# Kernel tuning notes

Measured on AMD Instinct MI355X. Metric: run time of the kernel, lower is better.

## Reference

```python
import jax, jax.numpy as jnp
import numpy as np

B, S, D = 8, 4096, 512
Q, C = 8, 1024


def setup_inputs() -> dict:
    key = jax.random.key(0)
    kx, kc = jax.random.split(key)
    x = jax.random.normal(kx, (B, S, D), dtype=jnp.float32)
    # learned codebooks for each residual quantizer level: [Q, C, D]
    codebooks = jax.random.normal(kc, (Q, C, D), dtype=jnp.float32)
    return {"x": x, "codebooks": codebooks}


def reference(x, codebooks):
    """Residual VQ: cascaded nearest-codebook lookups over residuals.

    Returns (quantized_out, indices [B,S,Q], commit_losses [Q]).
    """

    def step(carry, cb):
        residual, quant_out = carry
        # squared-distance argmin; ||r||^2 term is constant over codes, drop it
        # dist[b,s,c] ~ ||cb_c||^2 - 2 <r_bs, cb_c>
        dist = jnp.sum(cb * cb, axis=-1) - 2.0 * jnp.einsum("bsd,cd->bsc", residual, cb)
        idx = jnp.argmin(dist, axis=-1)            # [B, S]
        q = cb[idx]                                 # [B, S, D] gather
        commit = jnp.mean((jax.lax.stop_gradient(q) - residual) ** 2)
        # straight-through estimator
        q_st = residual + jax.lax.stop_gradient(q - residual)
        new_residual = residual - jax.lax.stop_gradient(q)
        return (new_residual, quant_out + q_st), (idx, commit)

    init = (x, jnp.zeros_like(x))
    (_, quantized), (indices, losses) = jax.lax.scan(step, init, codebooks)
    indices = jnp.transpose(indices, (1, 2, 0))  # [B, S, Q]
    return quantized, indices, losses
```

## Files before the change

### kernel.cpp

```cpp
#include <hip/hip_runtime.h>

#define BD 8
#define SD 4096
#define DDIM 512
#define QD 8
#define CDN 1024
#define ROWS (BD * SD)
#define QUANT_ELEMS (ROWS * DDIM)
#define IDX_OFF QUANT_ELEMS
#define LOSS_OFF (QUANT_ELEMS + ROWS * QD)

#define TPB 256
#define BR 32
#define MARGIN 0.25f

#define WS_LOSS 0
#define WS_FBCNT 64
#define WS_FBLIST 4096
#define WS_NORMS 0x40000
#define WS_PKHI 0x100000
#define WS_PKLO 0x900000
#define WS_RESID 0x1100000

typedef __attribute__((ext_vector_type(8))) short short8;
typedef __attribute__((ext_vector_type(4))) float f32x4;

__device__ __forceinline__ ushort f2bf(float x) {
    unsigned u = __float_as_uint(x);
    u += 0x7fff + ((u >> 16) & 1);
    return (ushort)(u >> 16);
}

__global__ __launch_bounds__(256) void vq_norms(const float* __restrict__ cb,
                                                float* __restrict__ norms) {
    int code = blockIdx.x * 4 + (threadIdx.x >> 6);
    int lane = threadIdx.x & 63;
    const float4* p = (const float4*)(cb + (size_t)code * DDIM);
    float4 a = p[lane];
    float4 b = p[lane + 64];
    float s = a.x * a.x + a.y * a.y + a.z * a.z + a.w * a.w +
              b.x * b.x + b.y * b.y + b.z * b.z + b.w * b.w;
#pragma unroll
    for (int m = 32; m >= 1; m >>= 1) s += __shfl_xor(s, m);
    if (lane == 0) norms[code] = s;
}

__global__ __launch_bounds__(256) void vq_cbpack(const float* __restrict__ cbs,
                                                 ushort* __restrict__ pkHi,
                                                 ushort* __restrict__ pkLo) {
    int sg = blockIdx.x * 256 + threadIdx.x;
    int lvl = sg >> 16;
    int s = sg & 65535;
    int tile = s >> 10;
    int kc = (s >> 6) & 15;
    int ln = s & 63;
    int code = tile * 16 + (ln & 15);
    int k0 = kc * 32 + (ln >> 4) * 8;
    const float* p = cbs + (size_t)lvl * CDN * DDIM + (size_t)code * DDIM + k0;
    float f[8];
    *(float4*)&f[0] = *(const float4*)p;
    *(float4*)&f[4] = *(const float4*)(p + 4);
    ushort h[8], l[8];
#pragma unroll
    for (int i = 0; i < 8; i++) {
        h[i] = f2bf(f[i]);
        float hf = __uint_as_float(((unsigned)h[i]) << 16);
        l[i] = f2bf(f[i] - hf);
    }
    *(short8*)(pkHi + (size_t)sg * 8) = *(short8*)h;
    *(short8*)(pkLo + (size_t)sg * 8) = *(short8*)l;
}

__global__ __launch_bounds__(TPB, 2) void vq_level_mfma(
    const float* __restrict__ rsrc, const float* __restrict__ qsub,
    float* __restrict__ resid, float* __restrict__ quant,
    const float* __restrict__ cbq, const float* __restrict__ normq,
    const ushort* __restrict__ pkHi, const ushort* __restrict__ pkLo,
    float* __restrict__ idx_out, double* __restrict__ lossq,
    int* __restrict__ fbCnt, int* __restrict__ fbList, int q) {
    __shared__ ushort Ah[BR * 512];
    __shared__ ushort Al[BR * 512];
    __shared__ float s_nrm[CDN];
    __shared__ float m_d1[4][BR], m_d2[4][BR], m_d3[4][BR];
    __shared__ int m_i1[4][BR], m_i2[4][BR];
    __shared__ int s_i1[BR], s_i2[BR], s_flag[BR];
    __shared__ double s_part[4];

    int tid = threadIdx.x;
    int lane = tid & 63;
    int l15 = lane & 15;
    int quad = lane >> 4;
    int cg = tid >> 6;
    int row0 = blockIdx.x * BR;

    for (int i = tid; i < CDN; i += TPB) s_nrm[i] = normq[i];

#pragma unroll
    for (int i = 0; i < 8; i++) {
        int flat = tid + TPB * i;
        int row = flat >> 6;
        int c = flat & 63;
        size_t g = (size_t)(row0 + row) * DDIM + c * 8;
        float f[8];
        *(float4*)&f[0] = *(const float4*)(rsrc + g);
        *(float4*)&f[4] = *(const float4*)(rsrc + g + 4);
        if (qsub) {
            float4 w0 = *(const float4*)(qsub + g);
            float4 w1 = *(const float4*)(qsub + g + 4);
            f[0] -= w0.x; f[1] -= w0.y; f[2] -= w0.z; f[3] -= w0.w;
            f[4] -= w1.x; f[5] -= w1.y; f[6] -= w1.z; f[7] -= w1.w;
        }
        ushort h[8], l[8];
#pragma unroll
        for (int k = 0; k < 8; k++) {
            h[k] = f2bf(f[k]);
            float hf = __uint_as_float(((unsigned)h[k]) << 16);
            l[k] = f2bf(f[k] - hf);
        }
        int dst = row * 512 + ((c ^ (row & 7)) * 8);
        *(short8*)(Ah + dst) = *(short8*)h;
        *(short8*)(Al + dst) = *(short8*)l;
    }
    __syncthreads();

    float td1[8], td2[8], td3[8];
    int ti1[8], ti2[8];
#pragma unroll
    for (int s = 0; s < 8; s++) { td1[s] = 3.4e38f; td2[s] = 3.4e38f; td3[s] = 3.4e38f; ti1[s] = 0; ti2[s] = 0; }

    short8 aR[2][4], bhR[2][4], blR[2][4];
    f32x4 acc[2][4];
    int aswz = l15 & 7;

#define LOADB(g, p) { int ct_ = (g) >> 4, kc_ = (g) & 15; \
    int base_ = ct_ * 131072 + cg * 32768 + kc_ * 512 + lane * 8; \
    _Pragma("unroll") for (int j = 0; j < 4; j++) { \
        bhR[p][j] = *(const short8*)(pkHi + base_ + j * 8192); \
        blR[p][j] = *(const short8*)(pkLo + base_ + j * 8192); } }

#define LOADA(g, p) { int c0_ = (((g) & 15) * 4 + quad) ^ aswz; \
    aR[p][0] = *(short8*)(Ah + l15 * 512 + c0_ * 8); \
    aR[p][1] = *(short8*)(Al + l15 * 512 + c0_ * 8); \
    aR[p][2] = *(short8*)(Ah + (16 + l15) * 512 + c0_ * 8); \
    aR[p][3] = *(short8*)(Al + (16 + l15) * 512 + c0_ * 8); }

#define BODY(g, p) { \
    if (((g) & 15) == 0) { \
        _Pragma("unroll") for (int rt = 0; rt < 2; rt++) \
        _Pragma("unroll") for (int j = 0; j < 4; j++) acc[rt][j] = (f32x4)0.0f; } \
    if ((g) < 63) { LOADB((g) + 1, 1 - (p)); LOADA((g) + 1, 1 - (p)); } \
    _Pragma("unroll") for (int j = 0; j < 4; j++) { \
        acc[0][j] = __builtin_amdgcn_mfma_f32_16x16x32_bf16(aR[p][0], bhR[p][j], acc[0][j], 0, 0, 0); \
        acc[0][j] = __builtin_amdgcn_mfma_f32_16x16x32_bf16(aR[p][1], bhR[p][j], acc[0][j], 0, 0, 0); \
        acc[0][j] = __builtin_amdgcn_mfma_f32_16x16x32_bf16(aR[p][0], blR[p][j], acc[0][j], 0, 0, 0); \
        acc[1][j] = __builtin_amdgcn_mfma_f32_16x16x32_bf16(aR[p][2], bhR[p][j], acc[1][j], 0, 0, 0); \
        acc[1][j] = __builtin_amdgcn_mfma_f32_16x16x32_bf16(aR[p][3], bhR[p][j], acc[1][j], 0, 0, 0); \
        acc[1][j] = __builtin_amdgcn_mfma_f32_16x16x32_bf16(aR[p][2], blR[p][j], acc[1][j], 0, 0, 0); } \
    if (((g) & 15) == 15) { int ct_ = (g) >> 4; \
        _Pragma("unroll") for (int j = 0; j < 4; j++) { \
            int code = (ct_ * 16 + cg * 4 + j) * 16 + l15; \
            float nrm = s_nrm[code]; \
            _Pragma("unroll") for (int rt = 0; rt < 2; rt++) \
            _Pragma("unroll") for (int reg = 0; reg < 4; reg++) { \
                float v = nrm - 2.0f * acc[rt][j][reg]; \
                int s = rt * 4 + reg; \
                bool b1 = v < td1[s]; bool b2 = v < td2[s]; bool b3 = v < td3[s]; \
                td3[s] = b2 ? td2[s] : (b3 ? v : td3[s]); \
                ti2[s] = b1 ? ti1[s] : (b2 ? code : ti2[s]); \
                td2[s] = b1 ? td1[s] : (b2 ? v : td2[s]); \
                ti1[s] = b1 ? code : ti1[s]; \
                td1[s] = b1 ? v : td1[s]; } } } }

    LOADB(0, 0); LOADA(0, 0);
    for (int gp = 0; gp < 32; gp++) {
        int g0 = gp * 2;
        BODY(g0, 0);
        BODY(g0 + 1, 1);
    }
#undef LOADB
#undef LOADA
#undef BODY

#pragma unroll
    for (int m = 1; m <= 8; m <<= 1) {
#pragma unroll
        for (int s = 0; s < 8; s++) {
            float o1 = __shfl_xor(td1[s], m); int oi1 = __shfl_xor(ti1[s], m);
            float o2 = __shfl_xor(td2[s], m); int oi2 = __shfl_xor(ti2[s], m);
            float o3 = __shfl_xor(td3[s], m);
            bool aw = (td1[s] < o1) || (td1[s] == o1 && ti1[s] < oi1);
            float w2 = aw ? td2[s] : o2; int wi2 = aw ? ti2[s] : oi2;
            float w3 = aw ? td3[s] : o3;
            float n1 = aw ? td1[s] : o1; int ni1 = aw ? ti1[s] : oi1;
            float p1 = aw ? o1 : td1[s]; int pi1 = aw ? oi1 : ti1[s];
            float p2 = aw ? o2 : td2[s];
            bool sw = (w2 < p1) || (w2 == p1 && wi2 < pi1);
            float n2 = sw ? w2 : p1; int ni2 = sw ? wi2 : pi1;
            float n3 = sw ? fminf(p1, w3) : fminf(w2, p2);
            td1[s] = n1; ti1[s] = ni1; td2[s] = n2; ti2[s] = ni2; td3[s] = n3;
        }
    }

    if (l15 == 0) {
#pragma unroll
        for (int s = 0; s < 8; s++) {
            int row = (s >> 2) * 16 + quad * 4 + (s & 3);
            m_d1[cg][row] = td1[s]; m_i1[cg][row] = ti1[s];
            m_d2[cg][row] = td2[s]; m_i2[cg][row] = ti2[s];
            m_d3[cg][row] = td3[s];
        }
    }
    __syncthreads();

    if (tid < BR) {
        int r = tid;
        float d1 = m_d1[0][r]; int i1 = m_i1[0][r];
        float d2 = m_d2[0][r]; int i2 = m_i2[0][r];
        float d3 = m_d3[0][r];
#pragma unroll
        for (int c = 1; c < 4; c++) {
            float o1 = m_d1[c][r]; int oi1 = m_i1[c][r];
            float o2 = m_d2[c][r]; int oi2 = m_i2[c][r];
            float o3 = m_d3[c][r];
            bool aw = (d1 < o1) || (d1 == o1 && i1 < oi1);
            float w2 = aw ? d2 : o2; int wi2 = aw ? i2 : oi2;
            float w3 = aw ? d3 : o3;
            float n1 = aw ? d1 : o1; int ni1 = aw ? i1 : oi1;
            float p1 = aw ? o1 : d1; int pi1 = aw ? oi1 : i1;
            float p2 = aw ? o2 : d2;
            bool sw = (w2 < p1) || (w2 == p1 && wi2 < pi1);
            float n2 = sw ? w2 : p1; int ni2 = sw ? wi2 : pi1;
            float n3 = sw ? fminf(p1, w3) : fminf(w2, p2);
            d1 = n1; i1 = ni1; d2 = n2; i2 = ni2; d3 = n3;
        }
        int flag = 0;
        if (d3 - d1 < MARGIN) flag = 2;
        else if (d2 - d1 < MARGIN) flag = 1;
        s_i1[r] = i1; s_i2[r] = i2; s_flag[r] = flag;
        if (flag == 2) {
            int p = atomicAdd(fbCnt, 1);
            if (p < 32768) fbList[p] = row0 + r;
        }
    }
    __syncthreads();

    for (int r = cg; r < BR; r += 4) {
        if (s_flag[r] != 1) continue;
        int i1 = s_i1[r], i2 = s_i2[r];
        size_t g = (size_t)(row0 + r) * DDIM + lane * 8;
        float rv[8];
        *(float4*)&rv[0] = *(const float4*)(rsrc + g);
        *(float4*)&rv[4] = *(const float4*)(rsrc + g + 4);
        if (qsub) {
            float4 w0 = *(const float4*)(qsub + g);
            float4 w1 = *(const float4*)(qsub + g + 4);
            rv[0] -= w0.x; rv[1] -= w0.y; rv[2] -= w0.z; rv[3] -= w0.w;
            rv[4] -= w1.x; rv[5] -= w1.y; rv[6] -= w1.z; rv[7] -= w1.w;
        }
        float c1[8], c2[8];
        *(float4*)&c1[0] = *(const float4*)(cbq + (size_t)i1 * DDIM + lane * 8);
        *(float4*)&c1[4] = *(const float4*)(cbq + (size_t)i1 * DDIM + lane * 8 + 4);
        *(float4*)&c2[0] = *(const float4*)(cbq + (size_t)i2 * DDIM + lane * 8);
        *(float4*)&c2[4] = *(const float4*)(cbq + (size_t)i2 * DDIM + lane * 8 + 4);
        float e1 = 0.0f, e2 = 0.0f;
#pragma unroll
        for (int i = 0; i < 8; i++) { e1 = fmaf(rv[i], c1[i], e1); e2 = fmaf(rv[i], c2[i], e2); }
#pragma unroll
        for (int m = 32; m >= 1; m >>= 1) { e1 += __shfl_xor(e1, m); e2 += __shfl_xor(e2, m); }
        float dd1 = s_nrm[i1] - 2.0f * e1;
        float dd2 = s_nrm[i2] - 2.0f * e2;
        bool take2 = (dd2 < dd1) || (dd2 == dd1 && i2 < i1);
        if (lane == 0) s_i1[r] = take2 ? i2 : i1;
    }
    __syncthreads();

    if (tid < BR) idx_out[(size_t)(row0 + tid) * QD + q] = (float)s_i1[tid];

    double ls = 0.0;
#pragma unroll 4
    for (int it = 0; it < 16; it++) {
        int flat = tid + TPB * it;
        int row = flat >> 7;
        int c4 = (flat & 127) * 4;
        if (s_flag[row] == 2) continue;
        size_t g = (size_t)(row0 + row) * DDIM + c4;
        float4 r = *(const float4*)(rsrc + g);
        if (qsub) {
            float4 w = *(const float4*)(qsub + g);
            r.x -= w.x; r.y -= w.y; r.z -= w.z; r.w -= w.w;
        }
        float4 cv = *(const float4*)(cbq + (size_t)s_i1[row] * DDIM + c4);
        float4 nr;
        nr.x = r.x - cv.x; nr.y = r.y - cv.y; nr.z = r.z - cv.z; nr.w = r.w - cv.w;
        if (resid) {
            *(float4*)(resid + g) = nr;
        } else {
            float4 qo = *(float4*)(quant + g);
            qo.x += cv.x; qo.y += cv.y; qo.z += cv.z; qo.w += cv.w;
            *(float4*)(quant + g) = qo;
        }
        ls += (double)nr.x * nr.x + (double)nr.y * nr.y +
              (double)nr.z * nr.z + (double)nr.w * nr.w;
    }
#pragma unroll
    for (int m = 32; m >= 1; m >>= 1) ls += __shfl_down(ls, m);
    if ((tid & 63) == 0) s_part[tid >> 6] = ls;
    __syncthreads();
    if (tid == 0) {
        double t = s_part[0] + s_part[1] + s_part[2] + s_part[3];
        atomicAdd(lossq, t);
    }
}

__global__ __launch_bounds__(256) void vq_fallback(
    const float* __restrict__ rsrc, const float* __restrict__ qsub,
    float* __restrict__ resid, float* __restrict__ quant,
    const float* __restrict__ cbq, const float* __restrict__ normq,
    float* __restrict__ idx_out, double* __restrict__ lossq,
    const int* __restrict__ fbCnt, const int* __restrict__ fbList, int q) {
    __shared__ float r_s[DDIM];
    __shared__ unsigned long long s_best;
    int tid = threadIdx.x;
    int n = *fbCnt; if (n > 32768) n = 32768;
    for (int w = blockIdx.x; w < n; w += gridDim.x) {
        int row = fbList[w];
        if (tid == 0) s_best = ~0ull;
        if (tid < 128) {
            size_t g = (size_t)row * DDIM + tid * 4;
            float4 v = *(const float4*)(rsrc + g);
            if (qsub) {
                float4 x = *(const float4*)(qsub + g);
                v.x -= x.x; v.y -= x.y; v.z -= x.z; v.w -= x.w;
            }
            *(float4*)&r_s[tid * 4] = v;
        }
        __syncthreads();
#pragma unroll
        for (int cc = 0; cc < 4; cc++) {
            int c = tid + 256 * cc;
            float dot = 0.0f;
            for (int k4 = 0; k4 < 128; k4++) {
                float4 cv = *(const float4*)(cbq + (size_t)c * DDIM + k4 * 4);
                float4 rv = *(const float4*)&r_s[k4 * 4];
                dot = fmaf(cv.x, rv.x, dot); dot = fmaf(cv.y, rv.y, dot);
                dot = fmaf(cv.z, rv.z, dot); dot = fmaf(cv.w, rv.w, dot);
            }
            float dist = normq[c] - 2.0f * dot;
            unsigned b = __float_as_uint(dist);
            b = (b & 0x80000000u) ? ~b : (b | 0x80000000u);
            unsigned long long key = (((unsigned long long)b) << 32) | (unsigned)c;
            atomicMin(&s_best, key);
        }
        __syncthreads();
        int idx = (int)(s_best & 0xffffffffull);
        if (tid == 0) idx_out[(size_t)row * QD + q] = (float)idx;
        double ls = 0.0;
        if (tid < 128) {
            size_t g = (size_t)row * DDIM + tid * 4;
            float4 r = *(const float4*)&r_s[tid * 4];
            float4 cv = *(const float4*)(cbq + (size_t)idx * DDIM + tid * 4);
            float4 nr;
            nr.x = r.x - cv.x; nr.y = r.y - cv.y; nr.z = r.z - cv.z; nr.w = r.w - cv.w;
            if (resid) {
                *(float4*)(resid + g) = nr;
            } else {
                float4 qo = *(float4*)(quant + g);
                qo.x += cv.x; qo.y += cv.y; qo.z += cv.z; qo.w += cv.w;
                *(float4*)(quant + g) = qo;
            }
            ls = (double)nr.x * nr.x + (double)nr.y * nr.y +
                 (double)nr.z * nr.z + (double)nr.w * nr.w;
        }
#pragma unroll
        for (int m = 32; m >= 1; m >>= 1) ls += __shfl_down(ls, m);
        if ((tid & 63) == 0 && ls != 0.0) atomicAdd(lossq, ls);
        __syncthreads();
    }
}

__global__ __launch_bounds__(256) void vq_quant_final(const float* __restrict__ x,
                                                      const float* __restrict__ resid,
                                                      float* __restrict__ quant) {
    size_t i = ((size_t)blockIdx.x * 256 + threadIdx.x) * 4;
    float4 xv = *(const float4*)(x + i);
    float4 rv = *(const float4*)(resid + i);
    float4 o;
    o.x = xv.x - rv.x; o.y = xv.y - rv.y; o.z = xv.z - rv.z; o.w = xv.w - rv.w;
    *(float4*)(quant + i) = o;
}

__global__ void vq_loss_final(const double* __restrict__ lossws, float* __restrict__ out) {
    int i = threadIdx.x;
    if (i < QD) out[i] = (float)(lossws[i] * (1.0 / (double)((size_t)ROWS * DDIM)));
}

extern "C" void kernel_launch(void* const* d_in, const int* in_sizes, int n_in,
                              void* d_out, int out_size, void* d_ws, size_t ws_size,
                              hipStream_t stream) {
    const float* x = (const float*)d_in[0];
    const float* cbs = (const float*)d_in[1];
    float* out = (float*)d_out;
    float* quant = out;
    float* idxo = out + IDX_OFF;
    float* losso = out + LOSS_OFF;

    char* ws = (char*)d_ws;
    double* lossws = (double*)(ws + WS_LOSS);
    int* fbCnt = (int*)(ws + WS_FBCNT);
    int* fbList = (int*)(ws + WS_FBLIST);
    float* norms = (float*)(ws + WS_NORMS);
    ushort* pkHi = (ushort*)(ws + WS_PKHI);
    ushort* pkLo = (ushort*)(ws + WS_PKLO);
    float* resid = (ws_size >= (size_t)WS_RESID + (size_t)QUANT_ELEMS * 4)
                       ? (float*)(ws + WS_RESID) : nullptr;

    hipMemsetAsync(d_ws, 0, 128, stream);
    if (!resid) hipMemsetAsync(d_out, 0, (size_t)out_size * 4, stream);

    vq_norms<<<QD * CDN / 4, 256, 0, stream>>>(cbs, norms);
    vq_cbpack<<<QD * 256, 256, 0, stream>>>(cbs, pkHi, pkLo);

    for (int q = 0; q < QD; q++) {
        const float* cbq = cbs + (size_t)q * CDN * DDIM;
        const float* nq = norms + (size_t)q * CDN;
        const ushort* pH = pkHi + (size_t)q * CDN * DDIM;
        const ushort* pL = pkLo + (size_t)q * CDN * DDIM;
        const float* rsrc;
        const float* qsubA;
        if (resid) {
            rsrc = (q == 0) ? x : resid;
            qsubA = nullptr;
        } else {
            rsrc = x;
            qsubA = quant;
        }
        vq_level_mfma<<<ROWS / BR, TPB, 0, stream>>>(
            rsrc, qsubA, resid, quant, cbq, nq, pH, pL,
            idxo, lossws + q, fbCnt + q, fbList, q);
        vq_fallback<<<128, 256, 0, stream>>>(
            rsrc, qsubA, resid, quant, cbq, nq, idxo, lossws + q,
            fbCnt + q, fbList, q);
    }
    if (resid) {
        vq_quant_final<<<QUANT_ELEMS / 1024, 256, 0, stream>>>(x, resid, quant);
    }
    vq_loss_final<<<1, 64, 0, stream>>>(lossws, losso);
}
```

Before: 1.784 ms.

## Use 8 waves per block and restructure MFMA loop over all code tiles

Doubles the block to 512 threads (8 waves), so each wave now covers half as many codes per tile. The main loop becomes K-outer over all four code tiles, keeping accumulators for every tile live and running the top-3 selection once at the end instead of per tile. This cuts B-operand loads per wave and reloads A fragments less often, aiming for more waves in flight and better latency hiding. In exchange it holds more accumulator registers, and the launch bound now asks for 4 blocks of 512 threads, which may force spills or limit occupancy.

After: 2.237 ms. 25.4% more time.

```diff
diff --git a/kernel.cpp b/kernel.cpp
--- a/kernel.cpp
+++ b/kernel.cpp
@@ -10,7 +10,8 @@
 #define IDX_OFF QUANT_ELEMS
 #define LOSS_OFF (QUANT_ELEMS + ROWS * QD)
 
-#define TPB 256
+#define TPB 512
+#define NWAVE (TPB / 64)
 #define BR 32
 #define MARGIN 0.25f
 
@@ -71,7 +72,7 @@
     *(short8*)(pkLo + (size_t)sg * 8) = *(short8*)l;
 }
 
-__global__ __launch_bounds__(TPB, 2) void vq_level_mfma(
+__global__ __launch_bounds__(TPB, 4) void vq_level_mfma(
     const float* __restrict__ rsrc, const float* __restrict__ qsub,
     float* __restrict__ resid, float* __restrict__ quant,
     const float* __restrict__ cbq, const float* __restrict__ normq,
@@ -81,10 +82,10 @@
     __shared__ ushort Ah[BR * 512];
     __shared__ ushort Al[BR * 512];
     __shared__ float s_nrm[CDN];
-    __shared__ float m_d1[4][BR], m_d2[4][BR], m_d3[4][BR];
-    __shared__ int m_i1[4][BR], m_i2[4][BR];
+    __shared__ float m_d1[NWAVE][BR], m_d2[NWAVE][BR], m_d3[NWAVE][BR];
+    __shared__ int m_i1[NWAVE][BR], m_i2[NWAVE][BR];
     __shared__ int s_i1[BR], s_i2[BR], s_flag[BR];
-    __shared__ double s_part[4];
+    __shared__ double s_part[NWAVE];
 
     int tid = threadIdx.x;
     int lane = tid & 63;
@@ -96,7 +97,7 @@
     for (int i = tid; i < CDN; i += TPB) s_nrm[i] = normq[i];
 
 #pragma unroll
-    for (int i = 0; i < 8; i++) {
+    for (int i = 0; i < 2048 / TPB; i++) {
         int flat = tid + TPB * i;
         int row = flat >> 6;
         int c = flat & 63;
@@ -128,58 +129,78 @@
 #pragma unroll
     for (int s = 0; s < 8; s++) { td1[s] = 3.4e38f; td2[s] = 3.4e38f; td3[s] = 3.4e38f; ti1[s] = 0; ti2[s] = 0; }
 
-    short8 aR[2][4], bhR[2][4], blR[2][4];
-    f32x4 acc[2][4];
+    short8 aR[2][4], bhR[2][2], blR[2][2];
+    f32x4 acc[2][4][2];
+#pragma unroll
+    for (int rt = 0; rt < 2; rt++)
+#pragma unroll
+        for (int ct = 0; ct < 4; ct++)
+#pragma unroll
+            for (int j = 0; j < 2; j++) acc[rt][ct][j] = (f32x4)0.0f;
     int aswz = l15 & 7;
 
-#define LOADB(g, p) { int ct_ = (g) >> 4, kc_ = (g) & 15; \
-    int base_ = ct_ * 131072 + cg * 32768 + kc_ * 512 + lane * 8; \
-    _Pragma("unroll") for (int j = 0; j < 4; j++) { \
-        bhR[p][j] = *(const short8*)(pkHi + base_ + j * 8192); \
-        blR[p][j] = *(const short8*)(pkLo + base_ + j * 8192); } }
-
-#define LOADA(g, p) { int c0_ = (((g) & 15) * 4 + quad) ^ aswz; \
+#define LOADB(g, p) { int kc_ = (g) >> 2, ct_ = (g) & 3; \
+    int base_ = ct_ * 131072 + cg * 16384 + kc_ * 512 + lane * 8; \
+    bhR[p][0] = *(const short8*)(pkHi + base_); \
+    blR[p][0] = *(const short8*)(pkLo + base_); \
+    bhR[p][1] = *(const short8*)(pkHi + base_ + 8192); \
+    blR[p][1] = *(const short8*)(pkLo + base_ + 8192); }
+
+#define LOADA(kc, p) { int c0_ = ((kc) * 4 + quad) ^ aswz; \
     aR[p][0] = *(short8*)(Ah + l15 * 512 + c0_ * 8); \
     aR[p][1] = *(short8*)(Al + l15 * 512 + c0_ * 8); \
     aR[p][2] = *(short8*)(Ah + (16 + l15) * 512 + c0_ * 8); \
     aR[p][3] = *(short8*)(Al + (16 + l15) * 512 + c0_ * 8); }
 
-#define BODY(g, p) { \
-    if (((g) & 15) == 0) { \
-        _Pragma("unroll") for (int rt = 0; rt < 2; rt++) \
-        _Pragma("unroll") for (int j = 0; j < 4; j++) acc[rt][j] = (f32x4)0.0f; } \
-    if ((g) < 63) { LOADB((g) + 1, 1 - (p)); LOADA((g) + 1, 1 - (p)); } \
-    _Pragma("unroll") for (int j = 0; j < 4; j++) { \
-        acc[0][j] = __builtin_amdgcn_mfma_f32_16x16x32_bf16(aR[p][0], bhR[p][j], acc[0][j], 0, 0, 0); \
-        acc[0][j] = __builtin_amdgcn_mfma_f32_16x16x32_bf16(aR[p][1], bhR[p][j], acc[0][j], 0, 0, 0); \
-        acc[0][j] = __builtin_amdgcn_mfma_f32_16x16x32_bf16(aR[p][0], blR[p][j], acc[0][j], 0, 0, 0); \
-        acc[1][j] = __builtin_amdgcn_mfma_f32_16x16x32_bf16(aR[p][2], bhR[p][j], acc[1][j], 0, 0, 0); \
-        acc[1][j] = __builtin_amdgcn_mfma_f32_16x16x32_bf16(aR[p][3], bhR[p][j], acc[1][j], 0, 0, 0); \
-        acc[1][j] = __builtin_amdgcn_mfma_f32_16x16x32_bf16(aR[p][2], blR[p][j], acc[1][j], 0, 0, 0); } \
-    if (((g) & 15) == 15) { int ct_ = (g) >> 4; \
-        _Pragma("unroll") for (int j = 0; j < 4; j++) { \
-            int code = (ct_ * 16 + cg * 4 + j) * 16 + l15; \
-            float nrm = s_nrm[code]; \
-            _Pragma("unroll") for (int rt = 0; rt < 2; rt++) \
-            _Pragma("unroll") for (int reg = 0; reg < 4; reg++) { \
-                float v = nrm - 2.0f * acc[rt][j][reg]; \
-                int s = rt * 4 + reg; \
-                bool b1 = v < td1[s]; bool b2 = v < td2[s]; bool b3 = v < td3[s]; \
-                td3[s] = b2 ? td2[s] : (b3 ? v : td3[s]); \
-                ti2[s] = b1 ? ti1[s] : (b2 ? code : ti2[s]); \
-                td2[s] = b1 ? td1[s] : (b2 ? v : td2[s]); \
-                ti1[s] = b1 ? code : ti1[s]; \
-                td1[s] = b1 ? v : td1[s]; } } } }
-
-    LOADB(0, 0); LOADA(0, 0);
-    for (int gp = 0; gp < 32; gp++) {
-        int g0 = gp * 2;
-        BODY(g0, 0);
-        BODY(g0 + 1, 1);
+#define STEP(g, CT, BP, AP, PA, kcA, apA) { \
+    LOADB((g) + 1, 1 - (BP)); \
+    if (PA) LOADA(kcA, apA); \
+    _Pragma("unroll") for (int j = 0; j < 2; j++) { \
+        acc[0][CT][j] = __builtin_amdgcn_mfma_f32_16x16x32_bf16(aR[AP][0], bhR[BP][j], acc[0][CT][j], 0, 0, 0); \
+        acc[0][CT][j] = __builtin_amdgcn_mfma_f32_16x16x32_bf16(aR[AP][1], bhR[BP][j], acc[0][CT][j], 0, 0, 0); \
+        acc[0][CT][j] = __builtin_amdgcn_mfma_f32_16x16x32_bf16(aR[AP][0], blR[BP][j], acc[0][CT][j], 0, 0, 0); \
+        acc[1][CT][j] = __builtin_amdgcn_mfma_f32_16x16x32_bf16(aR[AP][2], bhR[BP][j], acc[1][CT][j], 0, 0, 0); \
+        acc[1][CT][j] = __builtin_amdgcn_mfma_f32_16x16x32_bf16(aR[AP][3], bhR[BP][j], acc[1][CT][j], 0, 0, 0); \
+        acc[1][CT][j] = __builtin_amdgcn_mfma_f32_16x16x32_bf16(aR[AP][2], blR[BP][j], acc[1][CT][j], 0, 0, 0); } }
+
+    LOADB(0, 0);
+    LOADA(0, 0);
+    for (int kc2 = 0; kc2 < 8; kc2++) {
+        int g0 = kc2 * 8;
+        int nl = (kc2 < 7);
+        STEP(g0 + 0, 0, 0, 0, 1, 2 * kc2 + 1, 1);
+        STEP(g0 + 1, 1, 1, 0, 0, 0, 0);
+        STEP(g0 + 2, 2, 0, 0, 0, 0, 0);
+        STEP(g0 + 3, 3, 1, 0, 0, 0, 0);
+        STEP(g0 + 4, 0, 0, 1, nl, 2 * kc2 + 2, 0);
+        STEP(g0 + 5, 1, 1, 1, 0, 0, 0);
+        STEP(g0 + 6, 2, 0, 1, 0, 0, 0);
+        STEP(g0 + 7, 3, 1, 1, 0, 0, 0);
     }
 #undef LOADB
 #undef LOADA
-#undef BODY
+#undef STEP
+
+#pragma unroll
+    for (int ct = 0; ct < 4; ct++)
+#pragma unroll
+        for (int jj = 0; jj < 2; jj++) {
+            int code = (ct * 16 + cg * 2 + jj) * 16 + l15;
+            float nrm = s_nrm[code];
+#pragma unroll
+            for (int rt = 0; rt < 2; rt++)
+#pragma unroll
+                for (int reg = 0; reg < 4; reg++) {
+                    float v = nrm - 2.0f * acc[rt][ct][jj][reg];
+                    int s = rt * 4 + reg;
+                    bool b1 = v < td1[s]; bool b2 = v < td2[s]; bool b3 = v < td3[s];
+                    td3[s] = b2 ? td2[s] : (b3 ? v : td3[s]);
+                    ti2[s] = b1 ? ti1[s] : (b2 ? code : ti2[s]);
+                    td2[s] = b1 ? td1[s] : (b2 ? v : td2[s]);
+                    ti1[s] = b1 ? code : ti1[s];
+                    td1[s] = b1 ? v : td1[s];
+                }
+        }
 
 #pragma unroll
     for (int m = 1; m <= 8; m <<= 1) {
@@ -218,7 +239,7 @@
         float d2 = m_d2[0][r]; int i2 = m_i2[0][r];
         float d3 = m_d3[0][r];
 #pragma unroll
-        for (int c = 1; c < 4; c++) {
+        for (int c = 1; c < NWAVE; c++) {
             float o1 = m_d1[c][r]; int oi1 = m_i1[c][r];
             float o2 = m_d2[c][r]; int oi2 = m_i2[c][r];
             float o3 = m_d3[c][r];
@@ -244,7 +265,7 @@
     }
     __syncthreads();
 
-    for (int r = cg; r < BR; r += 4) {
+    for (int r = cg; r < BR; r += NWAVE) {
         if (s_flag[r] != 1) continue;
         int i1 = s_i1[r], i2 = s_i2[r];
         size_t g = (size_t)(row0 + r) * DDIM + lane * 8;
@@ -278,7 +299,7 @@
 
     double ls = 0.0;
 #pragma unroll 4
-    for (int it = 0; it < 16; it++) {
+    for (int it = 0; it < 4096 / TPB; it++) {
         int flat = tid + TPB * it;
         int row = flat >> 7;
         int c4 = (flat & 127) * 4;
@@ -307,7 +328,9 @@
     if ((tid & 63) == 0) s_part[tid >> 6] = ls;
     __syncthreads();
     if (tid == 0) {
-        double t = s_part[0] + s_part[1] + s_part[2] + s_part[3];
+        double t = 0.0;
+#pragma unroll
+        for (int i = 0; i < NWAVE; i++) t += s_part[i];
         atomicAdd(lossq, t);
     }
 }
```

## Replace split-bf16 triple MFMA with single fp16 MFMA and widen fallback margin

Applied to the files above, without the earlier changes.

Replaces the three-pass hi/lo bf16 MFMA distance computation with one fp16 MFMA pass. This cuts matrix work, codebook bandwidth and LDS footprint to roughly a third, and drops the lo-part packing. To absorb the larger fp16 rounding error, the near-tie margin that triggers exact fp32 re-checks rises from 0.25 to 0.75, so more rows go through the verification and fallback paths. The top-2 indices are also packed into one register per slot to lower register pressure.

Result: faster. 1.498 ms (-16.0%).

```diff
diff --git a/kernel.cpp b/kernel.cpp
--- a/kernel.cpp
+++ b/kernel.cpp
@@ -11,25 +11,20 @@
 #define LOSS_OFF (QUANT_ELEMS + ROWS * QD)
 
 #define TPB 256
+#define NWAVE (TPB / 64)
 #define BR 32
-#define MARGIN 0.25f
+#define MARGIN 0.75f
 
 #define WS_LOSS 0
 #define WS_FBCNT 64
 #define WS_FBLIST 4096
 #define WS_NORMS 0x40000
-#define WS_PKHI 0x100000
-#define WS_PKLO 0x900000
+#define WS_PK 0x100000
 #define WS_RESID 0x1100000
 
 typedef __attribute__((ext_vector_type(8))) short short8;
+typedef __attribute__((ext_vector_type(8))) _Float16 half8;
 typedef __attribute__((ext_vector_type(4))) float f32x4;
-
-__device__ __forceinline__ ushort f2bf(float x) {
-    unsigned u = __float_as_uint(x);
-    u += 0x7fff + ((u >> 16) & 1);
-    return (ushort)(u >> 16);
-}
 
 __global__ __launch_bounds__(256) void vq_norms(const float* __restrict__ cb,
                                                 float* __restrict__ norms) {
@@ -46,8 +41,7 @@
 }
 
 __global__ __launch_bounds__(256) void vq_cbpack(const float* __restrict__ cbs,
-                                                 ushort* __restrict__ pkHi,
-                                                 ushort* __restrict__ pkLo) {
+                                                 ushort* __restrict__ pk) {
     int sg = blockIdx.x * 256 + threadIdx.x;
     int lvl = sg >> 16;
     int s = sg & 65535;
@@ -60,31 +54,25 @@
     float f[8];
     *(float4*)&f[0] = *(const float4*)p;
     *(float4*)&f[4] = *(const float4*)(p + 4);
-    ushort h[8], l[8];
-#pragma unroll
-    for (int i = 0; i < 8; i++) {
-        h[i] = f2bf(f[i]);
-        float hf = __uint_as_float(((unsigned)h[i]) << 16);
-        l[i] = f2bf(f[i] - hf);
-    }
-    *(short8*)(pkHi + (size_t)sg * 8) = *(short8*)h;
-    *(short8*)(pkLo + (size_t)sg * 8) = *(short8*)l;
+    _Float16 h[8];
+#pragma unroll
+    for (int i = 0; i < 8; i++) h[i] = (_Float16)f[i];
+    *(short8*)(pk + (size_t)sg * 8) = *(short8*)h;
 }
 
 __global__ __launch_bounds__(TPB, 2) void vq_level_mfma(
     const float* __restrict__ rsrc, const float* __restrict__ qsub,
     float* __restrict__ resid, float* __restrict__ quant,
     const float* __restrict__ cbq, const float* __restrict__ normq,
-    const ushort* __restrict__ pkHi, const ushort* __restrict__ pkLo,
+    const ushort* __restrict__ pk,
     float* __restrict__ idx_out, double* __restrict__ lossq,
     int* __restrict__ fbCnt, int* __restrict__ fbList, int q) {
     __shared__ ushort Ah[BR * 512];
-    __shared__ ushort Al[BR * 512];
     __shared__ float s_nrm[CDN];
-    __shared__ float m_d1[4][BR], m_d2[4][BR], m_d3[4][BR];
-    __shared__ int m_i1[4][BR], m_i2[4][BR];
+    __shared__ float m_d1[NWAVE][BR], m_d2[NWAVE][BR], m_d3[NWAVE][BR];
+    __shared__ int m_i1[NWAVE][BR], m_i2[NWAVE][BR];
     __shared__ int s_i1[BR], s_i2[BR], s_flag[BR];
-    __shared__ double s_part[4];
+    __shared__ double s_part[NWAVE];
 
     int tid = threadIdx.x;
     int lane = tid & 63;
@@ -110,39 +98,31 @@
             f[0] -= w0.x; f[1] -= w0.y; f[2] -= w0.z; f[3] -= w0.w;
             f[4] -= w1.x; f[5] -= w1.y; f[6] -= w1.z; f[7] -= w1.w;
         }
-        ushort h[8], l[8];
-#pragma unroll
-        for (int k = 0; k < 8; k++) {
-            h[k] = f2bf(f[k]);
-            float hf = __uint_as_float(((unsigned)h[k]) << 16);
-            l[k] = f2bf(f[k] - hf);
-        }
+        _Float16 h[8];
+#pragma unroll
+        for (int k = 0; k < 8; k++) h[k] = (_Float16)f[k];
         int dst = row * 512 + ((c ^ (row & 7)) * 8);
         *(short8*)(Ah + dst) = *(short8*)h;
-        *(short8*)(Al + dst) = *(short8*)l;
     }
     __syncthreads();
 
     float td1[8], td2[8], td3[8];
-    int ti1[8], ti2[8];
-#pragma unroll
-    for (int s = 0; s < 8; s++) { td1[s] = 3.4e38f; td2[s] = 3.4e38f; td3[s] = 3.4e38f; ti1[s] = 0; ti2[s] = 0; }
-
-    short8 aR[2][4], bhR[2][4], blR[2][4];
+    int t12[8];
+#pragma unroll
+    for (int s = 0; s < 8; s++) { td1[s] = 3.4e38f; td2[s] = 3.4e38f; td3[s] = 3.4e38f; t12[s] = 0; }
+
+    half8 aR[2][2], bR[2][4];
     f32x4 acc[2][4];
     int aswz = l15 & 7;
 
 #define LOADB(g, p) { int ct_ = (g) >> 4, kc_ = (g) & 15; \
     int base_ = ct_ * 131072 + cg * 32768 + kc_ * 512 + lane * 8; \
-    _Pragma("unroll") for (int j = 0; j < 4; j++) { \
-        bhR[p][j] = *(const short8*)(pkHi + base_ + j * 8192); \
-        blR[p][j] = *(const short8*)(pkLo + base_ + j * 8192); } }
+    _Pragma("unroll") for (int j = 0; j < 4; j++) \
+        bR[p][j] = *(const half8*)(pk + base_ + j * 8192); }
 
 #define LOADA(g, p) { int c0_ = (((g) & 15) * 4 + quad) ^ aswz; \
-    aR[p][0] = *(short8*)(Ah + l15 * 512 + c0_ * 8); \
-    aR[p][1] = *(short8*)(Al + l15 * 512 + c0_ * 8); \
-    aR[p][2] = *(short8*)(Ah + (16 + l15) * 512 + c0_ * 8); \
-    aR[p][3] = *(short8*)(Al + (16 + l15) * 512 + c0_ * 8); }
+    aR[p][0] = *(half8*)(Ah + l15 * 512 + c0_ * 8); \
+    aR[p][1] = *(half8*)(Ah + (16 + l15) * 512 + c0_ * 8); }
 
 #define BODY(g, p) { \
     if (((g) & 15) == 0) { \
@@ -150,25 +130,22 @@
         _Pragma("unroll") for (int j = 0; j < 4; j++) acc[rt][j] = (f32x4)0.0f; } \
     if ((g) < 63) { LOADB((g) + 1, 1 - (p)); LOADA((g) + 1, 1 - (p)); } \
     _Pragma("unroll") for (int j = 0; j < 4; j++) { \
-        acc[0][j] = __builtin_amdgcn_mfma_f32_16x16x32_bf16(aR[p][0], bhR[p][j], acc[0][j], 0, 0, 0); \
-        acc[0][j] = __builtin_amdgcn_mfma_f32_16x16x32_bf16(aR[p][1], bhR[p][j], acc[0][j], 0, 0, 0); \
-        acc[0][j] = __builtin_amdgcn_mfma_f32_16x16x32_bf16(aR[p][0], blR[p][j], acc[0][j], 0, 0, 0); \
-        acc[1][j] = __builtin_amdgcn_mfma_f32_16x16x32_bf16(aR[p][2], bhR[p][j], acc[1][j], 0, 0, 0); \
-        acc[1][j] = __builtin_amdgcn_mfma_f32_16x16x32_bf16(aR[p][3], bhR[p][j], acc[1][j], 0, 0, 0); \
-        acc[1][j] = __builtin_amdgcn_mfma_f32_16x16x32_bf16(aR[p][2], blR[p][j], acc[1][j], 0, 0, 0); } \
+        acc[0][j] = __builtin_amdgcn_mfma_f32_16x16x32_f16(aR[p][0], bR[p][j], acc[0][j], 0, 0, 0); \
+        acc[1][j] = __builtin_amdgcn_mfma_f32_16x16x32_f16(aR[p][1], bR[p][j], acc[1][j], 0, 0, 0); } \
     if (((g) & 15) == 15) { int ct_ = (g) >> 4; \
         _Pragma("unroll") for (int j = 0; j < 4; j++) { \
-            int code = (ct_ * 16 + cg * 4 + j) * 16 + l15; \
-            float nrm = s_nrm[code]; \
+            int tile = ct_ * 16 + cg * 4 + j; \
+            float nrm = s_nrm[tile * 16 + l15]; \
             _Pragma("unroll") for (int rt = 0; rt < 2; rt++) \
             _Pragma("unroll") for (int reg = 0; reg < 4; reg++) { \
                 float v = nrm - 2.0f * acc[rt][j][reg]; \
                 int s = rt * 4 + reg; \
                 bool b1 = v < td1[s]; bool b2 = v < td2[s]; bool b3 = v < td3[s]; \
+                int pb1 = ((t12[s] & 63) << 6) | tile; \
+                int pb2 = (tile << 6) | (t12[s] & 63); \
                 td3[s] = b2 ? td2[s] : (b3 ? v : td3[s]); \
-                ti2[s] = b1 ? ti1[s] : (b2 ? code : ti2[s]); \
+                t12[s] = b1 ? pb1 : (b2 ? pb2 : t12[s]); \
                 td2[s] = b1 ? td1[s] : (b2 ? v : td2[s]); \
-                ti1[s] = b1 ? code : ti1[s]; \
                 td1[s] = b1 ? v : td1[s]; } } } }
 
     LOADB(0, 0); LOADA(0, 0);
@@ -180,6 +157,13 @@
 #undef LOADB
 #undef LOADA
 #undef BODY
+
+    int ti1[8], ti2[8];
+#pragma unroll
+    for (int s = 0; s < 8; s++) {
+        ti1[s] = (t12[s] & 63) * 16 + l15;
+        ti2[s] = ((t12[s] >> 6) & 63) * 16 + l15;
+    }
 
 #pragma unroll
     for (int m = 1; m <= 8; m <<= 1) {
@@ -218,7 +202,7 @@
         float d2 = m_d2[0][r]; int i2 = m_i2[0][r];
         float d3 = m_d3[0][r];
 #pragma unroll
-        for (int c = 1; c < 4; c++) {
+        for (int c = 1; c < NWAVE; c++) {
             float o1 = m_d1[c][r]; int oi1 = m_i1[c][r];
             float o2 = m_d2[c][r]; int oi2 = m_i2[c][r];
             float o3 = m_d3[c][r];
@@ -244,7 +228,7 @@
     }
     __syncthreads();
 
-    for (int r = cg; r < BR; r += 4) {
+    for (int r = cg; r < BR; r += NWAVE) {
         if (s_flag[r] != 1) continue;
         int i1 = s_i1[r], i2 = s_i2[r];
         size_t g = (size_t)(row0 + r) * DDIM + lane * 8;
@@ -409,8 +393,7 @@
     int* fbCnt = (int*)(ws + WS_FBCNT);
     int* fbList = (int*)(ws + WS_FBLIST);
     float* norms = (float*)(ws + WS_NORMS);
-    ushort* pkHi = (ushort*)(ws + WS_PKHI);
-    ushort* pkLo = (ushort*)(ws + WS_PKLO);
+    ushort* pk = (ushort*)(ws + WS_PK);
     float* resid = (ws_size >= (size_t)WS_RESID + (size_t)QUANT_ELEMS * 4)
                        ? (float*)(ws + WS_RESID) : nullptr;
 
@@ -418,13 +401,12 @@
     if (!resid) hipMemsetAsync(d_out, 0, (size_t)out_size * 4, stream);
 
     vq_norms<<<QD * CDN / 4, 256, 0, stream>>>(cbs, norms);
-    vq_cbpack<<<QD * 256, 256, 0, stream>>>(cbs, pkHi, pkLo);
+    vq_cbpack<<<QD * 256, 256, 0, stream>>>(cbs, pk);
 
     for (int q = 0; q < QD; q++) {
         const float* cbq = cbs + (size_t)q * CDN * DDIM;
         const float* nq = norms + (size_t)q * CDN;
-        const ushort* pH = pkHi + (size_t)q * CDN * DDIM;
-        const ushort* pL = pkLo + (size_t)q * CDN * DDIM;
+        const ushort* pq = pk + (size_t)q * CDN * DDIM;
         const float* rsrc;
         const float* qsubA;
         if (resid) {
@@ -435,7 +417,7 @@
             qsubA = quant;
         }
         vq_level_mfma<<<ROWS / BR, TPB, 0, stream>>>(
-            rsrc, qsubA, resid, quant, cbq, nq, pH, pL,
+            rsrc, qsubA, resid, quant, cbq, nq, pq,
             idxo, lossws + q, fbCnt + q, fbList, q);
         vq_fallback<<<128, 256, 0, stream>>>(
             rsrc, qsubA, resid, quant, cbq, nq, idxo, lossws + q,
```
